# Kernel optimization log

Hardware: AMD Instinct MI355X
Metric: run time of the kernel (lower is better)

## Reference

```python
import jax, jax.numpy as jnp
import numpy as np
from jax import lax

R = 4                 # radius (init kwarg)
EPS = 2.0             # eps (init kwarg)
K = 2 * R + 1         # stencil size


def _dir_kernels():
    """8 directional box kernels [8,1,K,K]: L,R,U,D,NW,NE,SW,SE (matches torch construction)."""
    base = np.ones((K, K), np.float32)
    L = base.copy(); L[:, R + 1:] = 0
    Rk = base.copy(); Rk[:, :R] = 0
    U = base.copy(); U[R + 1:, :] = 0
    D = base.copy(); D[:R, :] = 0
    NW = U.copy(); NE = U.copy(); SW = D.copy(); SE = D.copy()
    half = float((R + 1) * (2 * R + 1))
    L, Rk, U, D = L / half, Rk / half, U / half, D / half
    NW[:, R + 1:] = 0; NE[:, :R] = 0; SW[:, R + 1:] = 0; SE[:, :R] = 0
    quad = float((R + 1) ** 2)
    NW, NE, SW, SE = NW / quad, NE / quad, SW / quad, SE / quad
    return jnp.asarray(np.stack([L, Rk, U, D, NW, NE, SW, SE])[:, None])


def _pad(x):
    # ReplicationPad2d(R)
    return jnp.pad(x, ((0, 0), (0, 0), (R, R), (R, R)), mode='edge')


def _conv(x, w, groups=1):
    return lax.conv_general_dilated(
        x, w, window_strides=(1, 1), padding='VALID',
        dimension_numbers=('NCHW', 'OIHW', 'NCHW'), feature_group_count=groups)


def _resize_bilinear_ac(x, H, W):
    """Bilinear resize with align_corners=True, separable gather. x: [N,C,h,w]."""
    n, c, h, w = x.shape
    dt = x.dtype

    def coords(out, src):
        t = jnp.arange(out, dtype=dt) * (jnp.asarray(src - 1, dt) / jnp.asarray(out - 1, dt))
        i0 = jnp.clip(jnp.floor(t).astype(jnp.int32), 0, src - 2)
        f = t - i0.astype(dt)
        return i0, f

    y0, fy = coords(H, h)
    x0, fx = coords(W, w)
    rows = x[:, :, y0, :] * (1 - fy)[None, None, :, None] + x[:, :, y0 + 1, :] * fy[None, None, :, None]
    return rows[:, :, :, x0] * (1 - fx) + rows[:, :, :, x0 + 1] * fx


def setup_inputs() -> dict:
    key = jax.random.key(0)
    k1, k2, k3 = jax.random.split(key, 3)
    lr_x = jax.random.uniform(k1, (1, 3, 256, 256), jnp.float32) * 255.0
    lr_y = jax.random.uniform(k2, (1, 3, 256, 256), jnp.float32) * 255.0
    hr_x = jax.random.uniform(k3, (1, 3, 1024, 1024), jnp.float32) * 255.0
    box_w = jnp.full((3, 1, K, K), 1.0 / (K * K), jnp.float32)  # depthwise box filter weights
    return {"lr_x": lr_x, "lr_y": lr_y, "hr_x": hr_x, "box_w": box_w}


def reference(lr_x, lr_y, hr_x, box_w):
    H, W = hr_x.shape[2], hr_x.shape[3]
    box = lambda t: _conv(_pad(t), box_w, groups=3)

    # --- guided filter coefficients at low res ---
    mean_x = box(lr_x)
    mean_y = box(lr_y)
    cov_xy = box(lr_x * lr_y) - mean_x * mean_y
    var_x = box(lr_x * lr_x) - mean_x * mean_x
    A = cov_xy / (var_x + EPS)
    b = mean_y - A * mean_x

    # --- upsample A, b to hr (bilinear, align_corners=True) ---
    A = _resize_bilinear_ac(A, H, W)
    b = _resize_bilinear_ac(b, H, W)

    # --- 8-direction side-window stencil; channels treated as batch ---
    dirw = _dir_kernels()                      # [8,1,K,K]
    A3 = _pad(A.reshape(3, 1, H, W))
    b3 = _pad(b.reshape(3, 1, H, W))
    im3 = hr_x.reshape(3, 1, H, W)
    cA = _conv(A3, dirw)                       # [3,8,H,W]
    cB = _conv(b3, dirw)                       # [3,8,H,W]
    d = cA * im3 + cB - im3                    # [3,8,H,W]

    idx = jnp.argmin(jnp.abs(d), axis=1, keepdims=True)
    dm = jnp.take_along_axis(d, idx, axis=1)   # min-|delta| direction
    res = (dm + im3).reshape(1, 3, H, W)

    # res.int() truncates toward zero, then clamp(0,255), then float
    return jnp.clip(jnp.trunc(res), 0.0, 255.0)
```

## Files before the change

kernel.cpp:

```cpp
#include <hip/hip_runtime.h>

#define RR 4
#define LRH 256
#define LRW 256
#define HRH 1024
#define HRW 1024
#define TW 32
#define TH 8
#define GW (TW + 2*RR)
#define GH (TH + 2*RR)

__global__ __launch_bounds__(256) void lowres_coeffs(
    const float* __restrict__ lrx, const float* __restrict__ lry,
    float2* __restrict__ AB)
{
    __shared__ float4 sV[GH][GW];
    __shared__ float4 sH[GH][TW];

    const int c  = blockIdx.z;
    const int X0 = blockIdx.x * TW, Y0 = blockIdx.y * TH;
    const int tid = threadIdx.y * TW + threadIdx.x;
    const float* px = lrx + c * LRH * LRW;
    const float* py = lry + c * LRH * LRW;

    for (int i = tid; i < GH * GW; i += 256) {
        int r = i / GW, col = i - r * GW;
        int gy = min(max(Y0 - RR + r, 0), LRH - 1);
        int gx = min(max(X0 - RR + col, 0), LRW - 1);
        float xv = px[gy * LRW + gx];
        float yv = py[gy * LRW + gx];
        sV[r][col] = make_float4(xv, yv, xv * yv, xv * xv);
    }
    __syncthreads();

    for (int i = tid; i < GH * TW; i += 256) {
        int r = i / TW, col = i - r * TW;
        float4 s = sV[r][col];
        #pragma unroll
        for (int k = 1; k < 9; ++k) {
            float4 v = sV[r][col + k];
            s.x += v.x; s.y += v.y; s.z += v.z; s.w += v.w;
        }
        sH[r][col] = s;
    }
    __syncthreads();

    const int tx = threadIdx.x, ty = threadIdx.y;
    float4 s = sH[ty][tx];
    #pragma unroll
    for (int k = 1; k < 9; ++k) {
        float4 v = sH[ty + k][tx];
        s.x += v.x; s.y += v.y; s.z += v.z; s.w += v.w;
    }
    const float inv81 = 1.0f / 81.0f;
    float mx = s.x * inv81, my = s.y * inv81;
    float cov = s.z * inv81 - mx * my;
    float var = s.w * inv81 - mx * mx;
    float A = cov / (var + 2.0f);
    float B = my - A * mx;
    AB[(c * LRH + Y0 + ty) * LRW + X0 + tx] = make_float2(A, B);
}

__global__ __launch_bounds__(256) void stencil_kernel(
    const float2* __restrict__ AB,
    const float* __restrict__ hrx, float* __restrict__ out)
{
    __shared__ float2 sAB[GH][GW];
    __shared__ float4 sH[GH][TW];

    const int c  = blockIdx.z;
    const int X0 = blockIdx.x * TW, Y0 = blockIdx.y * TH;
    const int tid = threadIdx.y * TW + threadIdx.x;
    const float2* ABc = AB + c * LRH * LRW;
    const float scale = 255.0f / 1023.0f;

    for (int i = tid; i < GH * GW; i += 256) {
        int r = i / GW, col = i - r * GW;
        int gy = min(max(Y0 - RR + r, 0), HRH - 1);
        int gx = min(max(X0 - RR + col, 0), HRW - 1);
        float tyf = (float)gy * scale;
        int iy = (int)tyf; if (iy > LRH - 2) iy = LRH - 2;
        float fy = tyf - (float)iy;
        float txf = (float)gx * scale;
        int ix = (int)txf; if (ix > LRW - 2) ix = LRW - 2;
        float fx = txf - (float)ix;
        float2 v00 = ABc[iy * LRW + ix];
        float2 v01 = ABc[iy * LRW + ix + 1];
        float2 v10 = ABc[(iy + 1) * LRW + ix];
        float2 v11 = ABc[(iy + 1) * LRW + ix + 1];
        float a0 = v00.x * (1.0f - fy) + v10.x * fy;
        float a1 = v01.x * (1.0f - fy) + v11.x * fy;
        float b0 = v00.y * (1.0f - fy) + v10.y * fy;
        float b1 = v01.y * (1.0f - fy) + v11.y * fy;
        sAB[r][col] = make_float2(a0 * (1.0f - fx) + a1 * fx,
                                  b0 * (1.0f - fx) + b1 * fx);
    }
    __syncthreads();

    for (int i = tid; i < GH * TW; i += 256) {
        int r = i / TW, col = i - r * TW;
        float hLa = 0, hLb = 0, hRa = 0, hRb = 0;
        #pragma unroll
        for (int k = 0; k <= 4; ++k) {
            float2 v = sAB[r][col + k];
            hLa += v.x; hLb += v.y;
        }
        #pragma unroll
        for (int k = 4; k <= 8; ++k) {
            float2 v = sAB[r][col + k];
            hRa += v.x; hRb += v.y;
        }
        sH[r][col] = make_float4(hLa, hLb, hRa, hRb);
    }
    __syncthreads();

    const int tx = threadIdx.x, ty = threadIdx.y;
    float TLa=0,TLb=0,TRa=0,TRb=0, BLa=0,BLb=0,BRa=0,BRb=0;
    float Tca=0,Tcb=0, Bca=0,Bcb=0;
    float CLa=0,CLb=0,CRa=0,CRb=0, Cca=0,Ccb=0;
    #pragma unroll
    for (int k = 0; k < 9; ++k) {
        float4 h = sH[ty + k][tx];
        float2 cv = sAB[ty + k][tx + RR];
        if (k <= 4) { TLa+=h.x; TLb+=h.y; TRa+=h.z; TRb+=h.w; Tca+=cv.x; Tcb+=cv.y; }
        if (k >= 4) { BLa+=h.x; BLb+=h.y; BRa+=h.z; BRb+=h.w; Bca+=cv.x; Bcb+=cv.y; }
        if (k == 4) { CLa=h.x; CLb=h.y; CRa=h.z; CRb=h.w; Cca=cv.x; Ccb=cv.y; }
    }

    const int Y = Y0 + ty, X = X0 + tx;
    float xv = hrx[(c * HRH + Y) * HRW + X];
    const float i45 = 1.0f / 45.0f, i25 = 1.0f / 25.0f;
    float cA[8], cB[8];
    cA[0]=(TLa+BLa-CLa)*i45;      cB[0]=(TLb+BLb-CLb)*i45;
    cA[1]=(TRa+BRa-CRa)*i45;      cB[1]=(TRb+BRb-CRb)*i45;
    cA[2]=(TLa+TRa-Tca)*i45;      cB[2]=(TLb+TRb-Tcb)*i45;
    cA[3]=(BLa+BRa-Bca)*i45;      cB[3]=(BLb+BRb-Bcb)*i45;
    cA[4]=TLa*i25;                cB[4]=TLb*i25;
    cA[5]=TRa*i25;                cB[5]=TRb*i25;
    cA[6]=BLa*i25;                cB[6]=BLb*i25;
    cA[7]=BRa*i25;                cB[7]=BRb*i25;

    float best = 1e30f, bd = 0.f;
    #pragma unroll
    for (int i = 0; i < 8; ++i) {
        float d = cA[i] * xv + cB[i] - xv;
        float ad = fabsf(d);
        if (ad < best) { best = ad; bd = d; }
    }
    float res = truncf(bd + xv);
    res = fminf(fmaxf(res, 0.0f), 255.0f);
    out[(c * HRH + Y) * HRW + X] = res;
}

extern "C" void kernel_launch(void* const* d_in, const int* in_sizes, int n_in,
                              void* d_out, int out_size, void* d_ws, size_t ws_size,
                              hipStream_t stream) {
    const float* lrx = (const float*)d_in[0];
    const float* lry = (const float*)d_in[1];
    const float* hrx = (const float*)d_in[2];
    (void)d_in[3]; (void)in_sizes; (void)n_in; (void)out_size; (void)ws_size;

    float2* AB = (float2*)d_ws;
    float* outp = (float*)d_out;

    dim3 lgrid(LRW / TW, LRH / TH, 3);
    dim3 block(TW, TH);
    lowres_coeffs<<<lgrid, block, 0, stream>>>(lrx, lry, AB);

    dim3 grid(HRW / TW, HRH / TH, 3);
    stencil_kernel<<<grid, block, 0, stream>>>(AB, hrx, outp);
}
```

Baseline: 94.70 us.

## Use taller stencil tiles with multiple rows per thread and sliding vertical sums

The high-res stencil kernel now covers 32x32 tiles, and each thread computes 4 consecutive output rows. Vertical box sums are kept in registers and updated by a sliding window instead of being recomputed for every row. This cuts the halo overhead: bilinear upsampling of the guide coefficients drops from 16/8 rows loaded per output row to 40/32. It also means fewer shared-memory reads per output. In exchange it uses more registers per thread and more shared memory per block, which could lower occupancy.

```diff
diff --git a/kernel.cpp b/kernel.cpp
--- a/kernel.cpp
+++ b/kernel.cpp
@@ -5,26 +5,33 @@
 #define LRW 256
 #define HRH 1024
 #define HRW 1024
-#define TW 32
-#define TH 8
-#define GW (TW + 2*RR)
-#define GH (TH + 2*RR)
+
+#define LTW 32
+#define LTH 8
+#define LGW (LTW + 2*RR)
+#define LGH (LTH + 2*RR)
+
+#define STW 32
+#define STH 32
+#define RPT 4
+#define SGW (STW + 2*RR)
+#define SGH (STH + 2*RR)
 
 __global__ __launch_bounds__(256) void lowres_coeffs(
     const float* __restrict__ lrx, const float* __restrict__ lry,
     float2* __restrict__ AB)
 {
-    __shared__ float4 sV[GH][GW];
-    __shared__ float4 sH[GH][TW];
+    __shared__ float4 sV[LGH][LGW];
+    __shared__ float4 sH[LGH][LTW];
 
     const int c  = blockIdx.z;
-    const int X0 = blockIdx.x * TW, Y0 = blockIdx.y * TH;
-    const int tid = threadIdx.y * TW + threadIdx.x;
+    const int X0 = blockIdx.x * LTW, Y0 = blockIdx.y * LTH;
+    const int tid = threadIdx.y * LTW + threadIdx.x;
     const float* px = lrx + c * LRH * LRW;
     const float* py = lry + c * LRH * LRW;
 
-    for (int i = tid; i < GH * GW; i += 256) {
-        int r = i / GW, col = i - r * GW;
+    for (int i = tid; i < LGH * LGW; i += 256) {
+        int r = i / LGW, col = i - r * LGW;
         int gy = min(max(Y0 - RR + r, 0), LRH - 1);
         int gx = min(max(X0 - RR + col, 0), LRW - 1);
         float xv = px[gy * LRW + gx];
@@ -33,8 +40,8 @@
     }
     __syncthreads();
 
-    for (int i = tid; i < GH * TW; i += 256) {
-        int r = i / TW, col = i - r * TW;
+    for (int i = tid; i < LGH * LTW; i += 256) {
+        int r = i / LTW, col = i - r * LTW;
         float4 s = sV[r][col];
         #pragma unroll
         for (int k = 1; k < 9; ++k) {
@@ -65,17 +72,17 @@
     const float2* __restrict__ AB,
     const float* __restrict__ hrx, float* __restrict__ out)
 {
-    __shared__ float2 sAB[GH][GW];
-    __shared__ float4 sH[GH][TW];
+    __shared__ float2 sAB[SGH][SGW];
+    __shared__ float4 sH[SGH][STW];
 
     const int c  = blockIdx.z;
-    const int X0 = blockIdx.x * TW, Y0 = blockIdx.y * TH;
-    const int tid = threadIdx.y * TW + threadIdx.x;
+    const int X0 = blockIdx.x * STW, Y0 = blockIdx.y * STH;
+    const int tid = threadIdx.y * STW + threadIdx.x;
     const float2* ABc = AB + c * LRH * LRW;
     const float scale = 255.0f / 1023.0f;
 
-    for (int i = tid; i < GH * GW; i += 256) {
-        int r = i / GW, col = i - r * GW;
+    for (int i = tid; i < SGH * SGW; i += 256) {
+        int r = i / SGW, col = i - r * SGW;
         int gy = min(max(Y0 - RR + r, 0), HRH - 1);
         int gx = min(max(X0 - RR + col, 0), HRW - 1);
         float tyf = (float)gy * scale;
@@ -97,8 +104,8 @@
     }
     __syncthreads();
 
-    for (int i = tid; i < GH * TW; i += 256) {
-        int r = i / TW, col = i - r * TW;
+    for (int i = tid; i < SGH * STW; i += 256) {
+        int r = i / STW, col = i - r * STW;
         float hLa = 0, hLb = 0, hRa = 0, hRb = 0;
         #pragma unroll
         for (int k = 0; k <= 4; ++k) {
@@ -114,42 +121,67 @@
     }
     __syncthreads();
 
-    const int tx = threadIdx.x, ty = threadIdx.y;
-    float TLa=0,TLb=0,TRa=0,TRb=0, BLa=0,BLb=0,BRa=0,BRb=0;
-    float Tca=0,Tcb=0, Bca=0,Bcb=0;
-    float CLa=0,CLb=0,CRa=0,CRb=0, Cca=0,Ccb=0;
-    #pragma unroll
-    for (int k = 0; k < 9; ++k) {
-        float4 h = sH[ty + k][tx];
-        float2 cv = sAB[ty + k][tx + RR];
-        if (k <= 4) { TLa+=h.x; TLb+=h.y; TRa+=h.z; TRb+=h.w; Tca+=cv.x; Tcb+=cv.y; }
-        if (k >= 4) { BLa+=h.x; BLb+=h.y; BRa+=h.z; BRb+=h.w; Bca+=cv.x; Bcb+=cv.y; }
-        if (k == 4) { CLa=h.x; CLb=h.y; CRa=h.z; CRb=h.w; Cca=cv.x; Ccb=cv.y; }
-    }
-
-    const int Y = Y0 + ty, X = X0 + tx;
-    float xv = hrx[(c * HRH + Y) * HRW + X];
+    const int tx = threadIdx.x;
+    const int base = threadIdx.y * RPT;
+
+    float4 h[RPT + 8];
+    float2 cv[RPT + 8];
+    #pragma unroll
+    for (int k = 0; k < RPT + 8; ++k) {
+        h[k]  = sH[base + k][tx];
+        cv[k] = sAB[base + k][tx + RR];
+    }
+
+    float4 T = h[0], B = h[4];
+    float2 Tc = cv[0], Bc = cv[4];
+    #pragma unroll
+    for (int k = 1; k <= 4; ++k) {
+        T.x += h[k].x; T.y += h[k].y; T.z += h[k].z; T.w += h[k].w;
+        B.x += h[k+4].x; B.y += h[k+4].y; B.z += h[k+4].z; B.w += h[k+4].w;
+        Tc.x += cv[k].x; Tc.y += cv[k].y;
+        Bc.x += cv[k+4].x; Bc.y += cv[k+4].y;
+    }
+
     const float i45 = 1.0f / 45.0f, i25 = 1.0f / 25.0f;
-    float cA[8], cB[8];
-    cA[0]=(TLa+BLa-CLa)*i45;      cB[0]=(TLb+BLb-CLb)*i45;
-    cA[1]=(TRa+BRa-CRa)*i45;      cB[1]=(TRb+BRb-CRb)*i45;
-    cA[2]=(TLa+TRa-Tca)*i45;      cB[2]=(TLb+TRb-Tcb)*i45;
-    cA[3]=(BLa+BRa-Bca)*i45;      cB[3]=(BLb+BRb-Bcb)*i45;
-    cA[4]=TLa*i25;                cB[4]=TLb*i25;
-    cA[5]=TRa*i25;                cB[5]=TRb*i25;
-    cA[6]=BLa*i25;                cB[6]=BLb*i25;
-    cA[7]=BRa*i25;                cB[7]=BRb*i25;
-
-    float best = 1e30f, bd = 0.f;
-    #pragma unroll
-    for (int i = 0; i < 8; ++i) {
-        float d = cA[i] * xv + cB[i] - xv;
-        float ad = fabsf(d);
-        if (ad < best) { best = ad; bd = d; }
-    }
-    float res = truncf(bd + xv);
-    res = fminf(fmaxf(res, 0.0f), 255.0f);
-    out[(c * HRH + Y) * HRW + X] = res;
+    const int X = X0 + tx;
+
+    #pragma unroll
+    for (int j = 0; j < RPT; ++j) {
+        float4 C  = h[j + 4];
+        float2 Cc = cv[j + 4];
+        const int Y = Y0 + base + j;
+        float xv = hrx[(c * HRH + Y) * HRW + X];
+
+        float cA[8], cB[8];
+        cA[0] = (T.x + B.x - C.x) * i45;  cB[0] = (T.y + B.y - C.y) * i45;
+        cA[1] = (T.z + B.z - C.z) * i45;  cB[1] = (T.w + B.w - C.w) * i45;
+        cA[2] = (T.x + T.z - Tc.x) * i45; cB[2] = (T.y + T.w - Tc.y) * i45;
+        cA[3] = (B.x + B.z - Bc.x) * i45; cB[3] = (B.y + B.w - Bc.y) * i45;
+        cA[4] = T.x * i25;                cB[4] = T.y * i25;
+        cA[5] = T.z * i25;                cB[5] = T.w * i25;
+        cA[6] = B.x * i25;                cB[6] = B.y * i25;
+        cA[7] = B.z * i25;                cB[7] = B.w * i25;
+
+        float best = 1e30f, bd = 0.f;
+        #pragma unroll
+        for (int i = 0; i < 8; ++i) {
+            float d = cA[i] * xv + cB[i] - xv;
+            float ad = fabsf(d);
+            if (ad < best) { best = ad; bd = d; }
+        }
+        float res = truncf(bd + xv);
+        res = fminf(fmaxf(res, 0.0f), 255.0f);
+        out[(c * HRH + Y) * HRW + X] = res;
+
+        if (j < RPT - 1) {
+            T.x += h[j+5].x - h[j].x;   T.y += h[j+5].y - h[j].y;
+            T.z += h[j+5].z - h[j].z;   T.w += h[j+5].w - h[j].w;
+            B.x += h[j+9].x - h[j+4].x; B.y += h[j+9].y - h[j+4].y;
+            B.z += h[j+9].z - h[j+4].z; B.w += h[j+9].w - h[j+4].w;
+            Tc.x += cv[j+5].x - cv[j].x;   Tc.y += cv[j+5].y - cv[j].y;
+            Bc.x += cv[j+9].x - cv[j+4].x; Bc.y += cv[j+9].y - cv[j+4].y;
+        }
+    }
 }
 
 extern "C" void kernel_launch(void* const* d_in, const int* in_sizes, int n_in,
@@ -163,10 +195,11 @@
     float2* AB = (float2*)d_ws;
     float* outp = (float*)d_out;
 
-    dim3 lgrid(LRW / TW, LRH / TH, 3);
-    dim3 block(TW, TH);
-    lowres_coeffs<<<lgrid, block, 0, stream>>>(lrx, lry, AB);
-
-    dim3 grid(HRW / TW, HRH / TH, 3);
-    stencil_kernel<<<grid, block, 0, stream>>>(AB, hrx, outp);
+    dim3 lblock(LTW, LTH);
+    dim3 lgrid(LRW / LTW, LRH / LTH, 3);
+    lowres_coeffs<<<lgrid, lblock, 0, stream>>>(lrx, lry, AB);
+
+    dim3 sblock(STW, STH / RPT);
+    dim3 sgrid(HRW / STW, HRH / STH, 3);
+    stencil_kernel<<<sgrid, sblock, 0, stream>>>(AB, hrx, outp);
 }
```

Result: no change. 92.95 us (-1.8%).
